# Kernel tuning notes

Measured on AMD Instinct MI355X. Metric: run time of the kernel, lower is better.

The kernel has to match this reference:

```python
import jax, jax.numpy as jnp
import numpy as np

EPS = 1e-5
K_NN = 16

def _lin1d(x, W, b):
    # 1x1 Conv1d: x (B,C,N) -> (B,O,N)
    return jnp.einsum('oc,bcn->bon', W, x) + b[None, :, None]

def _lin2d(x, W, b):
    # 1x1 Conv2d: x (B,C,N,K) -> (B,O,N,K)
    return jnp.einsum('oc,bcnk->bonk', W, x) + b[None, :, None, None]

def _bn2d(x, gamma, beta):
    # train-mode BatchNorm2d over (B, N, K) per channel
    mean = jnp.mean(x, axis=(0, 2, 3), keepdims=True)
    var = jnp.var(x, axis=(0, 2, 3), keepdims=True)
    xh = (x - mean) * jax.lax.rsqrt(var + EPS)
    return gamma[None, :, None, None] * xh + beta[None, :, None, None]

def _knn_idx(pq, ps, k):
    # pq (B,3,N), ps (B,3,M) -> idx (B,N,K) of k nearest support points
    d2 = (jnp.sum(pq * pq, axis=1)[:, :, None]
          + jnp.sum(ps * ps, axis=1)[:, None, :]
          - 2.0 * jnp.einsum('bcn,bcm->bnm', pq, ps))
    _, idx = jax.lax.top_k(-d2, k)
    return idx

def _group(x, idx):
    # x (B,C,M), idx (B,N,K) -> (B,C,N,K)
    return jnp.take_along_axis(x[:, :, None, :], idx[:, None, :, :], axis=3)

def setup_inputs() -> dict:
    key = jax.random.key(0)
    ks = jax.random.split(key, 20)
    B, C, D, N, M, H = 4, 128, 64, 2048, 2048, 256
    s = lambda k, shape, scale: (jax.random.normal(k, shape, dtype=jnp.float32) * scale)
    return {
        'pq': s(ks[0], (B, 3, N), 1.0),
        'fq': s(ks[1], (B, C, N), 1.0),
        'ps': s(ks[2], (B, 3, M), 1.0),
        'fs': s(ks[3], (B, C, M), 1.0),
        'Wq': s(ks[4], (D, C), 0.05), 'bq': jnp.zeros((D,), jnp.float32),
        'Wk': s(ks[5], (D, C), 0.05), 'bk': jnp.zeros((D,), jnp.float32),
        'Wv': s(ks[6], (D, C), 0.05), 'bv': jnp.zeros((D,), jnp.float32),
        'Wp1': s(ks[7], (D, 3), 0.2), 'bp1': jnp.zeros((D,), jnp.float32),
        'gp': jnp.ones((D,), jnp.float32), 'btp': jnp.zeros((D,), jnp.float32),
        'Wp2': s(ks[8], (D, D), 0.05), 'bp2': jnp.zeros((D,), jnp.float32),
        'Wa1': s(ks[9], (H, D), 0.05), 'ba1': jnp.zeros((H,), jnp.float32),
        'ga': jnp.ones((H,), jnp.float32), 'bta': jnp.zeros((H,), jnp.float32),
        'Wa2': s(ks[10], (D, H), 0.05), 'ba2': jnp.zeros((D,), jnp.float32),
        'We': s(ks[11], (C, D), 0.05), 'be': jnp.zeros((C,), jnp.float32),
    }

def reference(pq, fq, ps, fs, Wq, bq, Wk, bk, Wv, bv,
              Wp1, bp1, gp, btp, Wp2, bp2,
              Wa1, ba1, ga, bta, Wa2, ba2, We, be):
    identity = fq
    q = _lin1d(fq, Wq, bq)          # (B,D,N)
    k = _lin1d(fs, Wk, bk)          # (B,D,M)
    v = _lin1d(fs, Wv, bv)          # (B,D,M)
    idx = _knn_idx(pq, ps, K_NN)    # (B,N,K)
    key_g = _group(k, idx)          # (B,D,N,K)
    qk_rel = q[:, :, :, None] - key_g
    pos_rel = pq[:, :, :, None] - _group(ps, idx)  # (B,3,N,K)
    # pos_mlp: conv-bn-relu-conv
    pe = _lin2d(pos_rel, Wp1, bp1)
    pe = jax.nn.relu(_bn2d(pe, gp, btp))
    pe = _lin2d(pe, Wp2, bp2)       # (B,D,N,K)
    # attn_mlp: conv-bn-relu-conv
    a = _lin2d(qk_rel + pe, Wa1, ba1)
    a = jax.nn.relu(_bn2d(a, ga, bta))
    a = _lin2d(a, Wa2, ba2)         # (B,D,N,K)
    attn = jax.nn.softmax(a, axis=-1)
    val = _group(v, idx) + pe       # (B,D,N,K)
    agg = jnp.einsum('bcnk,bcnk->bcn', attn, val)
    return _lin1d(agg, We, be) + identity
```

## Files before the change

### kernel.cpp

```cpp
#include <hip/hip_runtime.h>
#include <stdint.h>

#define NN 2048
#define MM 2048
#define NSAMP 131072

typedef float  fv4 __attribute__((ext_vector_type(4)));
typedef short  bfv8 __attribute__((ext_vector_type(8)));
typedef short  bfv4 __attribute__((ext_vector_type(4)));
typedef unsigned short u16;
typedef unsigned long long u64;

__device__ inline u16 f2bf(float x){
  unsigned u = __float_as_uint(x);
  return (u16)((u + 0x7FFFu + ((u>>16)&1u)) >> 16);
}
__device__ inline float bf2f(u16 u){ return __uint_as_float(((unsigned)u)<<16); }
#define MFMA16 __builtin_amdgcn_mfma_f32_16x16x32_bf16

__global__ __launch_bounds__(256) void k_prep(
    const float* __restrict__ Wq, const float* __restrict__ Wk, const float* __restrict__ Wv,
    const float* __restrict__ Wp2, const float* __restrict__ Wa2, const float* __restrict__ We,
    const float* __restrict__ ps,
    u16* __restrict__ Wqbf, u16* __restrict__ Wkbf, u16* __restrict__ Wvbf,
    u16* __restrict__ Wp2bf, u16* __restrict__ Wa2bf, u16* __restrict__ Webf,
    fv4* __restrict__ psP) {
  int gid = blockIdx.x * 256 + threadIdx.x;
  if (gid < 8192)  { Wqbf[gid] = f2bf(Wq[gid]); Wkbf[gid] = f2bf(Wk[gid]);
                     Wvbf[gid] = f2bf(Wv[gid]); Webf[gid] = f2bf(We[gid]); }
  if (gid < 4096)  Wp2bf[gid] = f2bf(Wp2[gid]);
  if (gid < 16384) Wa2bf[gid] = f2bf(Wa2[gid]);
  if (gid < 8192)  { int b = gid >> 11, m = gid & 2047;
    float x = ps[(b*3+0)*MM + m], y = ps[(b*3+1)*MM + m], z = ps[(b*3+2)*MM + m];
    fv4 p; p.x = x; p.y = y; p.z = z; p.w = x*x + y*y + z*z;
    psP[gid] = p; }
}

__global__ __launch_bounds__(256) void k_qkv(
    const float* __restrict__ fq, const float* __restrict__ fs,
    const u16* __restrict__ Wqbf, const u16* __restrict__ Wkbf, const u16* __restrict__ Wvbf,
    const float* __restrict__ bq, const float* __restrict__ bk, const float* __restrict__ bv,
    float* __restrict__ qT, float* __restrict__ kT, float* __restrict__ vT) {
  __shared__ u16 tile[2][32 * 136];
  int bid = blockIdx.x;
  int b = bid >> 6, p0 = (bid & 63) * 32;
  int t = threadIdx.x;
  int w = t >> 6, l = t & 63, lq = l >> 4, ln = l & 15;
  {
    int cq = t >> 3, n4 = (t & 7) * 4;
    #pragma unroll
    for (int it = 0; it < 4; ++it) {
      int c = it * 32 + cq;
      fv4 vq = *(const fv4*)&fq[(b*128 + c)*2048 + p0 + n4];
      fv4 vs = *(const fv4*)&fs[(b*128 + c)*2048 + p0 + n4];
      #pragma unroll
      for (int j = 0; j < 4; ++j) {
        tile[0][(n4 + j)*136 + c] = f2bf(vq[j]);
        tile[1][(n4 + j)*136 + c] = f2bf(vs[j]);
      }
    }
  }
  bfv8 A[3][4];
  #pragma unroll
  for (int mat = 0; mat < 3; ++mat) {
    const u16* W = mat == 0 ? Wqbf : (mat == 1 ? Wkbf : Wvbf);
    #pragma unroll
    for (int kk = 0; kk < 4; ++kk)
      A[mat][kk] = *(const bfv8*)(W + (w*16 + ln)*128 + kk*32 + lq*8);
  }
  __syncthreads();
  fv4 acc[3][2];
  #pragma unroll
  for (int mat = 0; mat < 3; ++mat) {
    const u16* tl = tile[mat == 0 ? 0 : 1];
    #pragma unroll
    for (int nt = 0; nt < 2; ++nt) {
      fv4 a = {0.f,0.f,0.f,0.f};
      #pragma unroll
      for (int kk = 0; kk < 4; ++kk) {
        bfv8 bb = *(const bfv8*)&tl[(nt*16 + ln)*136 + kk*32 + lq*8];
        a = MFMA16(A[mat][kk], bb, a, 0, 0, 0);
      }
      acc[mat][nt] = a;
    }
  }
  #pragma unroll
  for (int mat = 0; mat < 3; ++mat) {
    float* dst = mat == 0 ? qT : (mat == 1 ? kT : vT);
    const float* bia = mat == 0 ? bq : (mat == 1 ? bk : bv);
    fv4 bq4 = *(const fv4*)&bia[w*16 + lq*4];
    #pragma unroll
    for (int nt = 0; nt < 2; ++nt) {
      fv4 o = acc[mat][nt] + bq4;
      *(fv4*)&dst[(b*NN + p0 + nt*16 + ln)*64 + w*16 + lq*4] = o;
    }
  }
}

__global__ __launch_bounds__(256) void k_knn(
    const float* __restrict__ pq, const fv4* __restrict__ psP,
    int* __restrict__ idxb, float* __restrict__ posPart) {
  __shared__ u64 list[4][512];
  __shared__ u64 win[4][16];
  __shared__ int cnt[4];
  __shared__ float sacc[4][9];

  const int t = threadIdx.x, w = t >> 6, lane = t & 63;
  const int qi = blockIdx.x * 4 + w;
  const int b = qi >> 11, n = qi & 2047;
  const float* pqb = pq + b * 3 * NN;
  const fv4* psb = psP + b * 2048;
  const float qx = pqb[n], qy = pqb[NN + n], qz = pqb[2 * NN + n];
  const float qq = qx * qx + qy * qy + qz * qz;

  unsigned key[32];
  unsigned bkey = 0xFFFFFFFFu; unsigned bj = 0;
  #pragma unroll
  for (int j = 0; j < 32; ++j) {
    fv4 P = psb[lane + 64*j];
    float d2 = qq + P.w - 2.f * (qx * P.x + qy * P.y + qz * P.z);
    unsigned bu = __float_as_uint(d2);
    bu = (bu & 0x80000000u) ? ~bu : (bu | 0x80000000u);
    key[j] = bu;
    if (bu < bkey) { bkey = bu; bj = (unsigned)j; }
  }
  u64 e = (((u64)bkey) << 32) | (unsigned)(lane + 64*(int)bj);

  #pragma unroll
  for (int k = 2; k <= 64; k <<= 1) {
    #pragma unroll
    for (int j = k >> 1; j > 0; j >>= 1) {
      u64 x = __shfl_xor(e, j, 64);
      u64 lo = e < x ? e : x, hi = e < x ? x : e;
      bool up = ((lane & k) == 0);
      bool takeLo = (((lane & j) == 0) == up);
      e = takeLo ? lo : hi;
    }
  }
  const u64 thr = __shfl(e, 15, 64);
  const unsigned T32 = (unsigned)(thr >> 32);

  if (lane == 0) cnt[w] = 0;
  #pragma unroll
  for (int j = 0; j < 32; ++j) {
    if (key[j] <= T32) {
      int p = atomicAdd(&cnt[w], 1);
      if (p < 512) list[w][p] = (((u64)key[j]) << 32) | (unsigned)(lane + 64*j);
    }
  }
  const int C = *(volatile int*)&cnt[w];

  u64 myWin = 0;
  if (C <= 64) {
    u64 v = (lane < C) ? list[w][lane] : ~0ULL;
    #pragma unroll
    for (int k = 2; k <= 64; k <<= 1) {
      #pragma unroll
      for (int j = k >> 1; j > 0; j >>= 1) {
        u64 x = __shfl_xor(v, j, 64);
        u64 lo = v < x ? v : x, hi = v < x ? x : v;
        bool up = ((lane & k) == 0);
        bool takeLo = (((lane & j) == 0) == up);
        v = takeLo ? lo : hi;
      }
    }
    myWin = v;
  } else if (C <= 128) {
    u64 e0 = list[w][lane];
    u64 e1 = (64 + lane < C) ? list[w][64 + lane] : ~0ULL;
    #pragma unroll
    for (unsigned k = 2; k <= 128; k <<= 1) {
      #pragma unroll
      for (unsigned j = k >> 1; j > 0; j >>= 1) {
        if (j < 64) {
          u64 x0 = __shfl_xor(e0, (int)j, 64);
          u64 x1 = __shfl_xor(e1, (int)j, 64);
          bool lower = ((lane & j) == 0);
          bool up0 = (k == 128) ? true : ((lane & k) == 0);
          bool up1 = (k == 128) ? true : ((k == 64) ? false : ((lane & k) == 0));
          e0 = (lower == up0) ? (e0 < x0 ? e0 : x0) : (e0 < x0 ? x0 : e0);
          e1 = (lower == up1) ? (e1 < x1 ? e1 : x1) : (e1 < x1 ? x1 : e1);
        } else {
          u64 lo = e0 < e1 ? e0 : e1, hi = e0 < e1 ? e1 : e0;
          e0 = lo; e1 = hi;
        }
      }
    }
    myWin = e0;
  } else {
    int Cc = C > 512 ? 512 : C;
    for (int i = lane; i < 512; i += 64)
      if (i >= Cc) list[w][i] = ~0ULL;
    for (int r = 0; r < 16; ++r) {
      u64 mv = ~0ULL;
      #pragma unroll
      for (int s5 = 0; s5 < 8; ++s5) {
        u64 x = list[w][s5*64 + lane];
        mv = x < mv ? x : mv;
      }
      #pragma unroll
      for (int off = 1; off <= 32; off <<= 1) {
        u64 x = __shfl_xor(mv, off, 64);
        mv = x < mv ? x : mv;
      }
      #pragma unroll
      for (int s5 = 0; s5 < 8; ++s5)
        if (list[w][s5*64 + lane] == mv) list[w][s5*64 + lane] = ~0ULL;
      if (lane == 0) win[w][r] = mv;
    }
    if (lane < 16) myWin = win[w][lane];
  }

  if (lane < 16) {
    unsigned m = (unsigned)(myWin & 0xFFFFFFFFu);
    idxb[qi * 16 + lane] = (int)m;
    fv4 P = psb[m];
    float r0 = qx - P.x, r1 = qy - P.y, r2 = qz - P.z;
    float s[9];
    s[0] = r0; s[1] = r1; s[2] = r2;
    s[3] = r0*r0; s[4] = r0*r1; s[5] = r0*r2;
    s[6] = r1*r1; s[7] = r1*r2; s[8] = r2*r2;
    #pragma unroll
    for (int off = 1; off <= 8; off <<= 1)
      #pragma unroll
      for (int i = 0; i < 9; ++i) s[i] += __shfl_xor(s[i], off, 64);
    if (lane == 0)
      #pragma unroll
      for (int i = 0; i < 9; ++i) sacc[w][i] = s[i];
  }
  __syncthreads();
  if (t < 9) posPart[blockIdx.x * 12 + t]
      = sacc[0][t] + sacc[1][t] + sacc[2][t] + sacc[3][t];
}

__global__ __launch_bounds__(256) void k_posfinal(
    const float* __restrict__ Wp1, const float* __restrict__ bp1,
    const float* __restrict__ gp, const float* __restrict__ btp,
    const float* __restrict__ posPart, float* __restrict__ Wp1f, float* __restrict__ bp1f) {
  __shared__ float red[4][9];
  __shared__ float st[9];
  int t = threadIdx.x;
  int w = t >> 6, lane = t & 63;
  float s[9];
  #pragma unroll
  for (int i = 0; i < 9; ++i) s[i] = 0.f;
  #pragma unroll
  for (int it = 0; it < 8; ++it) {
    const float* p = posPart + (it * 256 + t) * 12;
    fv4 a = *(const fv4*)p;
    fv4 b4 = *(const fv4*)(p + 4);
    float c8 = p[8];
    s[0]+=a.x; s[1]+=a.y; s[2]+=a.z; s[3]+=a.w;
    s[4]+=b4.x; s[5]+=b4.y; s[6]+=b4.z; s[7]+=b4.w;
    s[8]+=c8;
  }
  #pragma unroll
  for (int off = 32; off > 0; off >>= 1)
    #pragma unroll
    for (int i = 0; i < 9; ++i) s[i] += __shfl_xor(s[i], off, 64);
  if (lane == 0)
    #pragma unroll
    for (int i = 0; i < 9; ++i) red[w][i] = s[i];
  __syncthreads();
  if (t < 9) st[t] = red[0][t] + red[1][t] + red[2][t] + red[3][t];
  __syncthreads();
  if (t < 64) {
    int d = t;
    const float invN = 1.f / (float)NSAMP;
    float m0 = st[0]*invN, m1 = st[1]*invN, m2 = st[2]*invN;
    float C00 = st[3]*invN - m0*m0, C01 = st[4]*invN - m0*m1, C02 = st[5]*invN - m0*m2;
    float C11 = st[6]*invN - m1*m1, C12 = st[7]*invN - m1*m2, C22 = st[8]*invN - m2*m2;
    float w0 = Wp1[d*3], w1 = Wp1[d*3+1], w2 = Wp1[d*3+2];
    float mean = w0*m0 + w1*m1 + w2*m2 + bp1[d];
    float var = w0*w0*C00 + w1*w1*C11 + w2*w2*C22 + 2.f*(w0*w1*C01 + w0*w2*C02 + w1*w2*C12);
    float scale = gp[d] * rsqrtf(var + 1e-5f);
    Wp1f[d*3]   = scale * w0;
    Wp1f[d*3+1] = scale * w1;
    Wp1f[d*3+2] = scale * w2;
    bp1f[d] = btp[d] + scale * (bp1[d] - mean);
  }
}

__global__ __launch_bounds__(256) void k_ystats(
    const float* __restrict__ pq, const float* __restrict__ ps,
    const float* __restrict__ qT, const float* __restrict__ kT,
    const int* __restrict__ idxb,
    const float* __restrict__ Wp1f, const float* __restrict__ bp1f,
    const u16* __restrict__ Wp2bf, const float* __restrict__ bp2,
    float* __restrict__ Gpart, float* __restrict__ ySumPart) {
  __shared__ __align__(16) unsigned char smem[21760];
  u16*   hp   = (u16*)smem;
  u16*   y2   = (u16*)(smem + 9216);
  float* r3   = (float*)(smem + 18432);
  float* qc   = (float*)(smem + 19200);
  int*   idxA = (int*)(smem + 20224);
  float* sWp1 = (float*)(smem + 20480);
  float* sbp1 = (float*)(smem + 21248);
  float* sbp2 = (float*)(smem + 21504);

  const int t = threadIdx.x;
  const int w = t >> 6, l = t & 63, lq = l >> 4, ln = l & 15;
  const int d0 = 16*w + lq*4;

  if (t < 192) sWp1[t] = Wp1f[t];
  if (t < 64){ sbp1[t] = bp1f[t]; sbp2[t] = bp2[t]; }

  bfv8 Ape[2];
  #pragma unroll
  for (int kk = 0; kk < 2; ++kk)
    Ape[kk] = *(const bfv8*)(Wp2bf + (16*w + ln)*64 + kk*32 + lq*8);

  fv4 gacc[4];
  #pragma unroll
  for (int nt = 0; nt < 4; ++nt) gacc[nt] = (fv4){0.f,0.f,0.f,0.f};
  float ys[4] = {0.f, 0.f, 0.f, 0.f};
  __syncthreads();

  for (int ch = 0; ch < 4; ++ch) {
    const int p0 = blockIdx.x * 16 + ch * 4;
    const int b  = p0 >> 11;
    const int bN = b * 2048;
    if (t < 64) idxA[t] = idxb[p0*16 + t];
    qc[t] = qT[(p0 + (t>>6))*64 + (t & 63)];
    __syncthreads();
    if (t < 192) { int c = t >> 6, s = t & 63; int n = (p0 + (s>>4)) & 2047;
      r3[c*64 + s] = pq[(b*3+c)*NN + n] - ps[(b*3+c)*MM + idxA[s]]; }
    __syncthreads();
    { int s = t >> 2, iq = t & 3;
      float r0 = r3[s], r1 = r3[64+s], r2 = r3[128+s];
      u16 tmp[16];
      #pragma unroll
      for (int e = 0; e < 16; ++e) { int i = iq*16 + e;
        float v = sbp1[i] + sWp1[i*3]*r0 + sWp1[i*3+1]*r1 + sWp1[i*3+2]*r2;
        tmp[e] = f2bf(fmaxf(v, 0.f)); }
      *(bfv8*)&hp[s*72 + iq*16]     = *(const bfv8*)&tmp[0];
      *(bfv8*)&hp[s*72 + iq*16 + 8] = *(const bfv8*)&tmp[8];
    }
    __syncthreads();
    {
      fv4 pe[4];
      #pragma unroll
      for (int nt = 0; nt < 4; ++nt) {
        fv4 acc = {0.f,0.f,0.f,0.f};
        #pragma unroll
        for (int kk = 0; kk < 2; ++kk) {
          bfv8 bb = *(const bfv8*)&hp[(nt*16 + ln)*72 + kk*32 + lq*8];
          acc = MFMA16(Ape[kk], bb, acc, 0, 0, 0);
        }
        pe[nt] = acc;
      }
      fv4 bp2q = *(const fv4*)&sbp2[d0];
      #pragma unroll
      for (int nt = 0; nt < 4; ++nt) {
        int s = nt*16 + ln;
        int mi = idxA[s];
        fv4 kg = *(const fv4*)(kT + (bN + mi)*64 + d0);
        fv4 qv = *(const fv4*)&qc[nt*64 + d0];
        fv4 yv = qv - kg + pe[nt] + bp2q;
        #pragma unroll
        for (int r = 0; r < 4; ++r) { y2[(d0 + r)*72 + s] = f2bf(yv[r]); ys[r] += yv[r]; }
      }
    }
    __syncthreads();
    #pragma unroll
    for (int kk = 0; kk < 2; ++kk) {
      bfv8 aa = *(const bfv8*)&y2[(16*w + ln)*72 + kk*32 + lq*8];
      #pragma unroll
      for (int nt = 0; nt < 4; ++nt) {
        bfv8 bb = *(const bfv8*)&y2[(nt*16 + ln)*72 + kk*32 + lq*8];
        gacc[nt] = MFMA16(aa, bb, gacc[nt], 0, 0, 0);
      }
    }
    __syncthreads();
  }
  #pragma unroll
  for (int nt = 0; nt < 4; ++nt)
    #pragma unroll
    for (int r = 0; r < 4; ++r)
      Gpart[blockIdx.x*4096 + (16*w + lq*4 + r)*64 + nt*16 + ln] = gacc[nt][r];
  #pragma unroll
  for (int off = 1; off <= 8; off <<= 1) {
    #pragma unroll
    for (int r = 0; r < 4; ++r) ys[r] += __shfl_xor(ys[r], off, 64);
  }
  if (ln == 0) {
    #pragma unroll
    for (int r = 0; r < 4; ++r) ySumPart[blockIdx.x*64 + d0 + r] = ys[r];
  }
}

__global__ __launch_bounds__(256) void k_gred(
    const float* __restrict__ Gpart, const float* __restrict__ ySumPart,
    float* __restrict__ G, float* __restrict__ ySum) {
  __shared__ float red[256];
  int bid = blockIdx.x, t = threadIdx.x;
  int tj = t & 63, st = t >> 6;
  if (bid < 64) {
    int j = bid * 64 + tj;
    float s = 0.f;
    for (int p = st * 128; p < st * 128 + 128; ++p)
      s += Gpart[p*4096 + j];
    red[st * 64 + tj] = s;
    __syncthreads();
    if (t < 64)
      G[bid * 64 + t] = red[t] + red[64 + t] + red[128 + t] + red[192 + t];
  } else {
    float s = 0.f;
    for (int p = st * 128; p < st * 128 + 128; ++p)
      s += ySumPart[p*64 + tj];
    red[st * 64 + tj] = s;
    __syncthreads();
    if (t < 64)
      ySum[t] = red[t] + red[64 + t] + red[128 + t] + red[192 + t];
  }
}

__global__ __launch_bounds__(256) void k_attnfinal(
    const float* __restrict__ Wa1, const float* __restrict__ ba1,
    const float* __restrict__ ga, const float* __restrict__ bta,
    const float* __restrict__ ySum, const float* __restrict__ G,
    u16* __restrict__ Wa1fbf, float* __restrict__ ba1f) {
  __shared__ float red[256];
  __shared__ float mu[64];
  __shared__ float sc[1];
  int h = blockIdx.x, t = threadIdx.x;
  const float invN = 1.f / (float)NSAMP;
  if (t < 64) mu[t] = ySum[t] * invN;
  __syncthreads();
  float acc = 0.f;
  #pragma unroll
  for (int e = 0; e < 16; ++e) {
    int pi = t*16 + e, i = pi >> 6, j = pi & 63;
    float cov = G[pi]*invN - mu[i]*mu[j];
    acc += Wa1[h*64 + i] * Wa1[h*64 + j] * cov;
  }
  red[t] = acc;
  __syncthreads();
  for (int s = 128; s > 0; s >>= 1) { if (t < s) red[t] += red[t + s]; __syncthreads(); }
  float var = red[0];
  __syncthreads();
  red[t] = (t < 64) ? Wa1[h*64 + t] * mu[t] : 0.f;
  __syncthreads();
  for (int s = 128; s > 0; s >>= 1) { if (t < s) red[t] += red[t + s]; __syncthreads(); }
  if (t == 0) {
    float mean  = red[0] + ba1[h];
    float scale = ga[h] * rsqrtf(var + 1e-5f);
    sc[0] = scale;
    ba1f[h] = bta[h] + scale * (ba1[h] - mean);
  }
  __syncthreads();
  if (t < 64) Wa1fbf[h*64 + t] = f2bf(sc[0] * Wa1[h*64 + t]);
}

__global__ __launch_bounds__(256) void k_main(
    const float* __restrict__ pq, const float* __restrict__ ps,
    const float* __restrict__ qT, const float* __restrict__ kT, const float* __restrict__ vT,
    const int* __restrict__ idxb,
    const float* __restrict__ Wp1f, const float* __restrict__ bp1f,
    const u16* __restrict__ Wp2bf, const float* __restrict__ bp2,
    const u16* __restrict__ Wa1fbf, const float* __restrict__ ba1f,
    const u16* __restrict__ Wa2bf, const float* __restrict__ ba2,
    const u16* __restrict__ Webf, const float* __restrict__ be,
    const float* __restrict__ fq,
    u16* __restrict__ aggbf, float* __restrict__ out) {
  __shared__ __align__(16) unsigned char smem[65024];
  u16*   hp   = (u16*)smem;
  u16*   ha   = (u16*)smem;
  u16*   ylds = (u16*)(smem + 33792);
  float* at   = (float*)(smem + 33792);
  u16*   vt   = (u16*)(smem + 51200);
  float* r3   = (float*)(smem + 60416);
  float* qc   = (float*)(smem + 61184);
  int*   idxA = (int*)(smem + 62208);
  float* sWp1 = (float*)(smem + 62464);
  float* sbp1 = (float*)(smem + 63232);
  float* sbp2 = (float*)(smem + 63488);
  float* sba1 = (float*)(smem + 63744);
  float* sba2 = (float*)(smem + 64768);

  const int t = threadIdx.x;
  const int w = t >> 6, l = t & 63, lq = l >> 4, ln = l & 15;
  const int d0 = 16*w + lq*4;

  if (t < 192) sWp1[t] = Wp1f[t];
  if (t < 64){ sbp1[t] = bp1f[t]; sbp2[t] = bp2[t]; sba2[t] = ba2[t]; }
  sba1[t] = ba1f[t];

  bfv8 Ape[2], A1[4][2], A2[8];
  #pragma unroll
  for (int kk = 0; kk < 2; ++kk)
    Ape[kk] = *(const bfv8*)(Wp2bf + (16*w + ln)*64 + kk*32 + lq*8);
  #pragma unroll
  for (int mt = 0; mt < 4; ++mt)
    #pragma unroll
    for (int kk = 0; kk < 2; ++kk)
      A1[mt][kk] = *(const bfv8*)(Wa1fbf + (64*w + mt*16 + ln)*64 + kk*32 + lq*8);
  #pragma unroll
  for (int kk = 0; kk < 8; ++kk)
    A2[kk] = *(const bfv8*)(Wa2bf + (16*w + ln)*256 + kk*32 + lq*8);
  __syncthreads();

  for (int ch = 0; ch < 4; ++ch) {
    const int p0 = blockIdx.x * 16 + ch * 4;
    const int b  = p0 >> 11;
    const int bN = b * 2048;
    if (t < 64) idxA[t] = idxb[p0*16 + t];
    qc[t] = qT[(p0 + (t>>6))*64 + (t & 63)];
    __syncthreads();
    if (t < 192) { int c = t >> 6, s = t & 63; int n = (p0 + (s>>4)) & 2047;
      r3[c*64 + s] = pq[(b*3+c)*NN + n] - ps[(b*3+c)*MM + idxA[s]]; }
    __syncthreads();
    { int s = t >> 2, iq = t & 3;
      float r0 = r3[s], r1 = r3[64+s], r2 = r3[128+s];
      u16 tmp[16];
      #pragma unroll
      for (int e = 0; e < 16; ++e) { int i = iq*16 + e;
        float v = sbp1[i] + sWp1[i*3]*r0 + sWp1[i*3+1]*r1 + sWp1[i*3+2]*r2;
        tmp[e] = f2bf(fmaxf(v, 0.f)); }
      *(bfv8*)&hp[s*72 + iq*16]     = *(const bfv8*)&tmp[0];
      *(bfv8*)&hp[s*72 + iq*16 + 8] = *(const bfv8*)&tmp[8];
    }
    __syncthreads();
    {
      fv4 pe[4];
      #pragma unroll
      for (int nt = 0; nt < 4; ++nt) {
        fv4 acc = {0.f,0.f,0.f,0.f};
        #pragma unroll
        for (int kk = 0; kk < 2; ++kk) {
          bfv8 bb = *(const bfv8*)&hp[(nt*16 + ln)*72 + kk*32 + lq*8];
          acc = MFMA16(Ape[kk], bb, acc, 0, 0, 0);
        }
        pe[nt] = acc;
      }
      fv4 bp2q = *(const fv4*)&sbp2[d0];
      #pragma unroll
      for (int nt = 0; nt < 4; ++nt) {
        int s = nt*16 + ln;
        int mi = idxA[s];
        fv4 kg = *(const fv4*)(kT + (bN + mi)*64 + d0);
        fv4 vg = *(const fv4*)(vT + (bN + mi)*64 + d0);
        fv4 qv = *(const fv4*)&qc[nt*64 + d0];
        fv4 pv = pe[nt] + bp2q;
        fv4 yv = qv - kg + pv;
        fv4 vv = vg + pv;
        u16 yp[4], vp[4];
        #pragma unroll
        for (int r = 0; r < 4; ++r) { yp[r] = f2bf(yv[r]); vp[r] = f2bf(vv[r]); }
        *(bfv4*)&ylds[s*72 + d0] = *(const bfv4*)yp;
        *(bfv4*)&vt[s*72 + d0]   = *(const bfv4*)vp;
      }
    }
    __syncthreads();
    #pragma unroll
    for (int nt = 0; nt < 4; ++nt) {
      int s = nt*16 + ln;
      bfv8 b0 = *(const bfv8*)&ylds[s*72 + lq*8];
      bfv8 b1 = *(const bfv8*)&ylds[s*72 + 32 + lq*8];
      #pragma unroll
      for (int mt = 0; mt < 4; ++mt) {
        fv4 acc = {0.f,0.f,0.f,0.f};
        acc = MFMA16(A1[mt][0], b0, acc, 0, 0, 0);
        acc = MFMA16(A1[mt][1], b1, acc, 0, 0, 0);
        int h0 = 64*w + mt*16 + lq*4;
        fv4 bq = *(const fv4*)&sba1[h0];
        u16 hv[4];
        #pragma unroll
        for (int r = 0; r < 4; ++r) hv[r] = f2bf(fmaxf(acc[r] + bq[r], 0.f));
        *(bfv4*)&ha[s*264 + h0] = *(const bfv4*)hv;
      }
    }
    __syncthreads();
    {
      fv4 acc2[4];
      #pragma unroll
      for (int nt = 0; nt < 4; ++nt) acc2[nt] = (fv4){0.f,0.f,0.f,0.f};
      #pragma unroll
      for (int kk = 0; kk < 8; ++kk) {
        #pragma unroll
        for (int nt = 0; nt < 4; ++nt) {
          bfv8 bb = *(const bfv8*)&ha[(nt*16 + ln)*264 + kk*32 + lq*8];
          acc2[nt] = MFMA16(A2[kk], bb, acc2[nt], 0, 0, 0);
        }
      }
      fv4 ba2q = *(const fv4*)&sba2[d0];
      #pragma unroll
      for (int nt = 0; nt < 4; ++nt) {
        int s = nt*16 + ln;
        fv4 o = acc2[nt] + ba2q;
        *(fv4*)&at[s*68 + d0] = o;
      }
    }
    __syncthreads();
    {
      int dd = t & 63, pt = t >> 6;
      float a[16];
      #pragma unroll
      for (int k = 0; k < 16; ++k) a[k] = at[(pt*16 + k)*68 + dd];
      float mx = a[0];
      #pragma unroll
      for (int k = 1; k < 16; ++k) mx = fmaxf(mx, a[k]);
      float sum = 0.f, num = 0.f;
      #pragma unroll
      for (int k = 0; k < 16; ++k) {
        float e = __expf(a[k] - mx);
        sum += e;
        num += e * bf2f(vt[(pt*16 + k)*72 + dd]);
      }
      aggbf[(p0 + pt)*64 + dd] = f2bf(num / sum);
    }
    __syncthreads();
  }
  {
    const int P0 = blockIdx.x * 16;
    const int b  = P0 >> 11;
    const int n0 = P0 & 2047;
    bfv8 EA[2][2];
    #pragma unroll
    for (int mt = 0; mt < 2; ++mt)
      #pragma unroll
      for (int kk = 0; kk < 2; ++kk)
        EA[mt][kk] = *(const bfv8*)(Webf + ((w*2 + mt)*16 + ln)*64 + kk*32 + lq*8);
    const u16* bp = aggbf + (P0 + ln)*64;
    bfv8 b0 = *(const bfv8*)(bp + lq*8);
    bfv8 b1 = *(const bfv8*)(bp + 32 + lq*8);
    fv4 eacc[2];
    #pragma unroll
    for (int mt = 0; mt < 2; ++mt) {
      fv4 a = {0.f,0.f,0.f,0.f};
      a = MFMA16(EA[mt][0], b0, a, 0, 0, 0);
      a = MFMA16(EA[mt][1], b1, a, 0, 0, 0);
      eacc[mt] = a;
    }
    #pragma unroll
    for (int mt = 0; mt < 2; ++mt) {
      int c0 = (w*2 + mt)*16 + lq*4;
      fv4 bev = *(const fv4*)&be[c0];
      #pragma unroll
      for (int r = 0; r < 4; ++r) {
        int c = c0 + r;
        int o = (b*128 + c)*2048 + n0 + ln;
        out[o] = eacc[mt][r] + bev[r] + fq[o];
      }
    }
  }
}

extern "C" void kernel_launch(void* const* d_in, const int* in_sizes, int n_in,
                              void* d_out, int out_size, void* d_ws, size_t ws_size,
                              hipStream_t stream) {
  (void)in_sizes; (void)n_in; (void)out_size; (void)ws_size;
  const float* pq  = (const float*)d_in[0];
  const float* fq  = (const float*)d_in[1];
  const float* ps  = (const float*)d_in[2];
  const float* fs  = (const float*)d_in[3];
  const float* Wq  = (const float*)d_in[4];  const float* bq  = (const float*)d_in[5];
  const float* Wk  = (const float*)d_in[6];  const float* bk  = (const float*)d_in[7];
  const float* Wv  = (const float*)d_in[8];  const float* bv  = (const float*)d_in[9];
  const float* Wp1 = (const float*)d_in[10]; const float* bp1 = (const float*)d_in[11];
  const float* gp  = (const float*)d_in[12]; const float* btp = (const float*)d_in[13];
  const float* Wp2 = (const float*)d_in[14]; const float* bp2 = (const float*)d_in[15];
  const float* Wa1 = (const float*)d_in[16]; const float* ba1 = (const float*)d_in[17];
  const float* ga  = (const float*)d_in[18]; const float* bta = (const float*)d_in[19];
  const float* Wa2 = (const float*)d_in[20]; const float* ba2 = (const float*)d_in[21];
  const float* We  = (const float*)d_in[22]; const float* be  = (const float*)d_in[23];
  float* ws = (float*)d_ws;
  float* qT    = ws;
  float* kT    = ws + 524288;
  float* vT    = ws + 1048576;
  u16*   aggbf = (u16*)(ws + 1572864);
  int*   idxb  = (int*)(ws + 2097152);
  u16*   Wqbf  = (u16*)(ws + 2228224);
  u16*   Wkbf  = (u16*)(ws + 2232320);
  u16*   Wvbf  = (u16*)(ws + 2236416);
  u16*   Webf  = (u16*)(ws + 2240512);
  fv4*   psP   = (fv4*)(ws + 2244608);
  float* Wp1f  = ws + 2375680;
  float* bp1f  = ws + 2375872;
  float* ba1f  = ws + 2375936;
  float* G     = ws + 2376192;
  float* ySum  = ws + 2380288;
  float* ySumP = ws + 2380352;
  u16*   Wp2bf  = (u16*)(ws + 2413120);
  u16*   Wa2bf  = (u16*)(ws + 2415168);
  u16*   Wa1fbf = (u16*)(ws + 2423360);
  float* posPart = ws + 2431552;
  float* Gpart   = ws + 2480704;
  float* out   = (float*)d_out;

  k_prep<<<64, 256, 0, stream>>>(Wq, Wk, Wv, Wp2, Wa2, We, ps,
                                 Wqbf, Wkbf, Wvbf, Wp2bf, Wa2bf, Webf, psP);
  k_qkv<<<256, 256, 0, stream>>>(fq, fs, Wqbf, Wkbf, Wvbf, bq, bk, bv, qT, kT, vT);
  k_knn<<<2048, 256, 0, stream>>>(pq, psP, idxb, posPart);
  k_posfinal<<<1, 256, 0, stream>>>(Wp1, bp1, gp, btp, posPart, Wp1f, bp1f);
  k_ystats<<<512, 256, 0, stream>>>(pq, ps, qT, kT, idxb, Wp1f, bp1f, Wp2bf, bp2,
                                    Gpart, ySumP);
  k_gred<<<65, 256, 0, stream>>>(Gpart, ySumP, G, ySum);
  k_attnfinal<<<256, 256, 0, stream>>>(Wa1, ba1, ga, bta, ySum, G, Wa1fbf, ba1f);
  k_main<<<512, 256, 0, stream>>>(pq, ps, qT, kT, vT, idxb, Wp1f, bp1f, Wp2bf, bp2,
                                  Wa1fbf, ba1f, Wa2bf, ba2, Webf, be, fq, aggbf, out);
}
```

Measured before the change: 213.3 us.

## Materialize grouped y and value tensors in ystats; slim k_main to consume them

k_ystats now also gathers v, adds the positional encoding, and writes both the attention input y and the value tensor as bf16 to global workspace. k_main no longer recomputes the position MLP and gathers, and reads these tensors directly. It does the softmax in registers with shuffles instead of through shared memory, and uses a much smaller LDS footprint with launch bounds for higher occupancy. k_ystats runs twice as many blocks with half the points each. The trade is about 32MB of extra global write and read traffic in exchange for removing duplicated compute and LDS round trips.

```diff
diff --git a/kernel.cpp b/kernel.cpp
--- a/kernel.cpp
+++ b/kernel.cpp
@@ -283,10 +283,11 @@
 
 __global__ __launch_bounds__(256) void k_ystats(
     const float* __restrict__ pq, const float* __restrict__ ps,
-    const float* __restrict__ qT, const float* __restrict__ kT,
+    const float* __restrict__ qT, const float* __restrict__ kT, const float* __restrict__ vT,
     const int* __restrict__ idxb,
     const float* __restrict__ Wp1f, const float* __restrict__ bp1f,
     const u16* __restrict__ Wp2bf, const float* __restrict__ bp2,
+    u16* __restrict__ yg, u16* __restrict__ valg,
     float* __restrict__ Gpart, float* __restrict__ ySumPart) {
   __shared__ __align__(16) unsigned char smem[21760];
   u16*   hp   = (u16*)smem;
@@ -316,8 +317,8 @@
   float ys[4] = {0.f, 0.f, 0.f, 0.f};
   __syncthreads();
 
-  for (int ch = 0; ch < 4; ++ch) {
-    const int p0 = blockIdx.x * 16 + ch * 4;
+  for (int ch = 0; ch < 2; ++ch) {
+    const int p0 = blockIdx.x * 8 + ch * 4;
     const int b  = p0 >> 11;
     const int bN = b * 2048;
     if (t < 64) idxA[t] = idxb[p0*16 + t];
@@ -355,10 +356,20 @@
         int s = nt*16 + ln;
         int mi = idxA[s];
         fv4 kg = *(const fv4*)(kT + (bN + mi)*64 + d0);
+        fv4 vg = *(const fv4*)(vT + (bN + mi)*64 + d0);
         fv4 qv = *(const fv4*)&qc[nt*64 + d0];
-        fv4 yv = qv - kg + pe[nt] + bp2q;
+        fv4 pv = pe[nt] + bp2q;
+        fv4 yv = qv - kg + pv;
+        fv4 vv = vg + pv;
+        u16 yp[4], vp[4];
         #pragma unroll
-        for (int r = 0; r < 4; ++r) { y2[(d0 + r)*72 + s] = f2bf(yv[r]); ys[r] += yv[r]; }
+        for (int r = 0; r < 4; ++r) {
+          yp[r] = f2bf(yv[r]); vp[r] = f2bf(vv[r]);
+          y2[(d0 + r)*72 + s] = yp[r];
+          ys[r] += yv[r];
+        }
+        *(bfv4*)&yg[((u64)(p0 + nt)*16 + ln)*64 + d0]   = *(const bfv4*)yp;
+        *(bfv4*)&valg[((u64)(p0 + nt)*16 + ln)*64 + d0] = *(const bfv4*)vp;
       }
     }
     __syncthreads();
@@ -398,7 +409,7 @@
   if (bid < 64) {
     int j = bid * 64 + tj;
     float s = 0.f;
-    for (int p = st * 128; p < st * 128 + 128; ++p)
+    for (int p = st * 256; p < st * 256 + 256; ++p)
       s += Gpart[p*4096 + j];
     red[st * 64 + tj] = s;
     __syncthreads();
@@ -406,7 +417,7 @@
       G[bid * 64 + t] = red[t] + red[64 + t] + red[128 + t] + red[192 + t];
   } else {
     float s = 0.f;
-    for (int p = st * 128; p < st * 128 + 128; ++p)
+    for (int p = st * 256; p < st * 256 + 256; ++p)
       s += ySumPart[p*64 + tj];
     red[st * 64 + tj] = s;
     __syncthreads();
@@ -452,44 +463,20 @@
   if (t < 64) Wa1fbf[h*64 + t] = f2bf(sc[0] * Wa1[h*64 + t]);
 }
 
-__global__ __launch_bounds__(256) void k_main(
-    const float* __restrict__ pq, const float* __restrict__ ps,
-    const float* __restrict__ qT, const float* __restrict__ kT, const float* __restrict__ vT,
-    const int* __restrict__ idxb,
-    const float* __restrict__ Wp1f, const float* __restrict__ bp1f,
-    const u16* __restrict__ Wp2bf, const float* __restrict__ bp2,
+__global__ __launch_bounds__(256, 4) void k_main(
+    const u16* __restrict__ yg, const u16* __restrict__ valg,
     const u16* __restrict__ Wa1fbf, const float* __restrict__ ba1f,
     const u16* __restrict__ Wa2bf, const float* __restrict__ ba2,
     const u16* __restrict__ Webf, const float* __restrict__ be,
     const float* __restrict__ fq,
     u16* __restrict__ aggbf, float* __restrict__ out) {
-  __shared__ __align__(16) unsigned char smem[65024];
-  u16*   hp   = (u16*)smem;
-  u16*   ha   = (u16*)smem;
-  u16*   ylds = (u16*)(smem + 33792);
-  float* at   = (float*)(smem + 33792);
-  u16*   vt   = (u16*)(smem + 51200);
-  float* r3   = (float*)(smem + 60416);
-  float* qc   = (float*)(smem + 61184);
-  int*   idxA = (int*)(smem + 62208);
-  float* sWp1 = (float*)(smem + 62464);
-  float* sbp1 = (float*)(smem + 63232);
-  float* sbp2 = (float*)(smem + 63488);
-  float* sba1 = (float*)(smem + 63744);
-  float* sba2 = (float*)(smem + 64768);
+  __shared__ __align__(16) u16 ha[64 * 264];
 
   const int t = threadIdx.x;
   const int w = t >> 6, l = t & 63, lq = l >> 4, ln = l & 15;
   const int d0 = 16*w + lq*4;
 
-  if (t < 192) sWp1[t] = Wp1f[t];
-  if (t < 64){ sbp1[t] = bp1f[t]; sbp2[t] = bp2[t]; sba2[t] = ba2[t]; }
-  sba1[t] = ba1f[t];
-
-  bfv8 Ape[2], A1[4][2], A2[8];
-  #pragma unroll
-  for (int kk = 0; kk < 2; ++kk)
-    Ape[kk] = *(const bfv8*)(Wp2bf + (16*w + ln)*64 + kk*32 + lq*8);
+  bfv8 A1[4][2], A2[8];
   #pragma unroll
   for (int mt = 0; mt < 4; ++mt)
     #pragma unroll
@@ -498,72 +485,27 @@
   #pragma unroll
   for (int kk = 0; kk < 8; ++kk)
     A2[kk] = *(const bfv8*)(Wa2bf + (16*w + ln)*256 + kk*32 + lq*8);
-  __syncthreads();
+  fv4 bq1[4];
+  #pragma unroll
+  for (int mt = 0; mt < 4; ++mt)
+    bq1[mt] = *(const fv4*)&ba1f[64*w + mt*16 + lq*4];
+  const fv4 ba2q = *(const fv4*)&ba2[d0];
 
   for (int ch = 0; ch < 4; ++ch) {
     const int p0 = blockIdx.x * 16 + ch * 4;
-    const int b  = p0 >> 11;
-    const int bN = b * 2048;
-    if (t < 64) idxA[t] = idxb[p0*16 + t];
-    qc[t] = qT[(p0 + (t>>6))*64 + (t & 63)];
-    __syncthreads();
-    if (t < 192) { int c = t >> 6, s = t & 63; int n = (p0 + (s>>4)) & 2047;
-      r3[c*64 + s] = pq[(b*3+c)*NN + n] - ps[(b*3+c)*MM + idxA[s]]; }
-    __syncthreads();
-    { int s = t >> 2, iq = t & 3;
-      float r0 = r3[s], r1 = r3[64+s], r2 = r3[128+s];
-      u16 tmp[16];
-      #pragma unroll
-      for (int e = 0; e < 16; ++e) { int i = iq*16 + e;
-        float v = sbp1[i] + sWp1[i*3]*r0 + sWp1[i*3+1]*r1 + sWp1[i*3+2]*r2;
-        tmp[e] = f2bf(fmaxf(v, 0.f)); }
-      *(bfv8*)&hp[s*72 + iq*16]     = *(const bfv8*)&tmp[0];
-      *(bfv8*)&hp[s*72 + iq*16 + 8] = *(const bfv8*)&tmp[8];
-    }
-    __syncthreads();
-    {
-      fv4 pe[4];
-      #pragma unroll
-      for (int nt = 0; nt < 4; ++nt) {
-        fv4 acc = {0.f,0.f,0.f,0.f};
-        #pragma unroll
-        for (int kk = 0; kk < 2; ++kk) {
-          bfv8 bb = *(const bfv8*)&hp[(nt*16 + ln)*72 + kk*32 + lq*8];
-          acc = MFMA16(Ape[kk], bb, acc, 0, 0, 0);
-        }
-        pe[nt] = acc;
-      }
-      fv4 bp2q = *(const fv4*)&sbp2[d0];
-      #pragma unroll
-      for (int nt = 0; nt < 4; ++nt) {
-        int s = nt*16 + ln;
-        int mi = idxA[s];
-        fv4 kg = *(const fv4*)(kT + (bN + mi)*64 + d0);
-        fv4 vg = *(const fv4*)(vT + (bN + mi)*64 + d0);
-        fv4 qv = *(const fv4*)&qc[nt*64 + d0];
-        fv4 pv = pe[nt] + bp2q;
-        fv4 yv = qv - kg + pv;
-        fv4 vv = vg + pv;
-        u16 yp[4], vp[4];
-        #pragma unroll
-        for (int r = 0; r < 4; ++r) { yp[r] = f2bf(yv[r]); vp[r] = f2bf(vv[r]); }
-        *(bfv4*)&ylds[s*72 + d0] = *(const bfv4*)yp;
-        *(bfv4*)&vt[s*72 + d0]   = *(const bfv4*)vp;
-      }
-    }
-    __syncthreads();
     #pragma unroll
     for (int nt = 0; nt < 4; ++nt) {
+      const u16* yp = yg + ((u64)(p0 + nt)*16 + ln)*64;
+      bfv8 b0 = *(const bfv8*)(yp + lq*8);
+      bfv8 b1 = *(const bfv8*)(yp + 32 + lq*8);
       int s = nt*16 + ln;
-      bfv8 b0 = *(const bfv8*)&ylds[s*72 + lq*8];
-      bfv8 b1 = *(const bfv8*)&ylds[s*72 + 32 + lq*8];
       #pragma unroll
       for (int mt = 0; mt < 4; ++mt) {
         fv4 acc = {0.f,0.f,0.f,0.f};
         acc = MFMA16(A1[mt][0], b0, acc, 0, 0, 0);
         acc = MFMA16(A1[mt][1], b1, acc, 0, 0, 0);
         int h0 = 64*w + mt*16 + lq*4;
-        fv4 bq = *(const fv4*)&sba1[h0];
+        fv4 bq = bq1[mt];
         u16 hv[4];
         #pragma unroll
         for (int r = 0; r < 4; ++r) hv[r] = f2bf(fmaxf(acc[r] + bq[r], 0.f));
@@ -571,43 +513,46 @@
       }
     }
     __syncthreads();
-    {
-      fv4 acc2[4];
-      #pragma unroll
-      for (int nt = 0; nt < 4; ++nt) acc2[nt] = (fv4){0.f,0.f,0.f,0.f};
-      #pragma unroll
-      for (int kk = 0; kk < 8; ++kk) {
+    fv4 acc2[4];
+    #pragma unroll
+    for (int nt = 0; nt < 4; ++nt) acc2[nt] = (fv4){0.f,0.f,0.f,0.f};
+    #pragma unroll
+    for (int kk = 0; kk < 8; ++kk) {
+      #pragma unroll
+      for (int nt = 0; nt < 4; ++nt) {
+        bfv8 bb = *(const bfv8*)&ha[(nt*16 + ln)*264 + kk*32 + lq*8];
+        acc2[nt] = MFMA16(A2[kk], bb, acc2[nt], 0, 0, 0);
+      }
+    }
+    #pragma unroll
+    for (int nt = 0; nt < 4; ++nt) {
+      fv4 a = acc2[nt] + ba2q;
+      fv4 m = a;
+      #pragma unroll
+      for (int off = 1; off <= 8; off <<= 1)
         #pragma unroll
-        for (int nt = 0; nt < 4; ++nt) {
-          bfv8 bb = *(const bfv8*)&ha[(nt*16 + ln)*264 + kk*32 + lq*8];
-          acc2[nt] = MFMA16(A2[kk], bb, acc2[nt], 0, 0, 0);
+        for (int r = 0; r < 4; ++r) m[r] = fmaxf(m[r], __shfl_xor(m[r], off, 16));
+      fv4 ee, num;
+      bfv4 vv4 = *(const bfv4*)(valg + ((u64)(p0 + nt)*16 + ln)*64 + d0);
+      #pragma unroll
+      for (int r = 0; r < 4; ++r) {
+        ee[r] = __expf(a[r] - m[r]);
+        num[r] = ee[r] * bf2f((u16)vv4[r]);
+      }
+      fv4 sum = ee;
+      #pragma unroll
+      for (int off = 1; off <= 8; off <<= 1)
+        #pragma unroll
+        for (int r = 0; r < 4; ++r) {
+          sum[r] += __shfl_xor(sum[r], off, 16);
+          num[r] += __shfl_xor(num[r], off, 16);
         }
-      }
-      fv4 ba2q = *(const fv4*)&sba2[d0];
-      #pragma unroll
-      for (int nt = 0; nt < 4; ++nt) {
-        int s = nt*16 + ln;
-        fv4 o = acc2[nt] + ba2q;
-        *(fv4*)&at[s*68 + d0] = o;
-      }
-    }
-    __syncthreads();
-    {
-      int dd = t & 63, pt = t >> 6;
-      float a[16];
-      #pragma unroll
-      for (int k = 0; k < 16; ++k) a[k] = at[(pt*16 + k)*68 + dd];
-      float mx = a[0];
-      #pragma unroll
-      for (int k = 1; k < 16; ++k) mx = fmaxf(mx, a[k]);
-      float sum = 0.f, num = 0.f;
-      #pragma unroll
-      for (int k = 0; k < 16; ++k) {
-        float e = __expf(a[k] - mx);
-        sum += e;
-        num += e * bf2f(vt[(pt*16 + k)*72 + dd]);
-      }
-      aggbf[(p0 + pt)*64 + dd] = f2bf(num / sum);
+      if (ln == 0) {
+        u16 o[4];
+        #pragma unroll
+        for (int r = 0; r < 4; ++r) o[r] = f2bf(num[r] / sum[r]);
+        *(bfv4*)&aggbf[(u64)(p0 + nt)*64 + d0] = *(const bfv4*)o;
+      }
     }
     __syncthreads();
   }
@@ -669,23 +614,25 @@
   float* kT    = ws + 524288;
   float* vT    = ws + 1048576;
   u16*   aggbf = (u16*)(ws + 1572864);
-  int*   idxb  = (int*)(ws + 2097152);
-  u16*   Wqbf  = (u16*)(ws + 2228224);
-  u16*   Wkbf  = (u16*)(ws + 2232320);
-  u16*   Wvbf  = (u16*)(ws + 2236416);
-  u16*   Webf  = (u16*)(ws + 2240512);
-  fv4*   psP   = (fv4*)(ws + 2244608);
-  float* Wp1f  = ws + 2375680;
-  float* bp1f  = ws + 2375872;
-  float* ba1f  = ws + 2375936;
-  float* G     = ws + 2376192;
-  float* ySum  = ws + 2380288;
-  float* ySumP = ws + 2380352;
-  u16*   Wp2bf  = (u16*)(ws + 2413120);
-  u16*   Wa2bf  = (u16*)(ws + 2415168);
-  u16*   Wa1fbf = (u16*)(ws + 2423360);
-  float* posPart = ws + 2431552;
-  float* Gpart   = ws + 2480704;
+  int*   idxb  = (int*)(ws + 1835008);
+  u16*   Wqbf  = (u16*)(ws + 1966080);
+  u16*   Wkbf  = (u16*)(ws + 1970176);
+  u16*   Wvbf  = (u16*)(ws + 1974272);
+  u16*   Webf  = (u16*)(ws + 1978368);
+  fv4*   psP   = (fv4*)(ws + 1982464);
+  float* Wp1f  = ws + 2015232;
+  float* bp1f  = ws + 2015424;
+  float* ba1f  = ws + 2015488;
+  float* G     = ws + 2015744;
+  float* ySum  = ws + 2019840;
+  float* ySumP = ws + 2019904;
+  u16*   Wp2bf  = (u16*)(ws + 2085440);
+  u16*   Wa2bf  = (u16*)(ws + 2087488);
+  u16*   Wa1fbf = (u16*)(ws + 2095680);
+  float* posPart = ws + 2103872;
+  float* Gpart   = ws + 2128448;
+  u16*   yg    = (u16*)(ws + 6322752);
+  u16*   valg  = (u16*)(ws + 10517056);
   float* out   = (float*)d_out;
 
   k_prep<<<64, 256, 0, stream>>>(Wq, Wk, Wv, Wp2, Wa2, We, ps,
@@ -693,10 +640,10 @@
   k_qkv<<<256, 256, 0, stream>>>(fq, fs, Wqbf, Wkbf, Wvbf, bq, bk, bv, qT, kT, vT);
   k_knn<<<2048, 256, 0, stream>>>(pq, psP, idxb, posPart);
   k_posfinal<<<1, 256, 0, stream>>>(Wp1, bp1, gp, btp, posPart, Wp1f, bp1f);
-  k_ystats<<<512, 256, 0, stream>>>(pq, ps, qT, kT, idxb, Wp1f, bp1f, Wp2bf, bp2,
-                                    Gpart, ySumP);
+  k_ystats<<<1024, 256, 0, stream>>>(pq, ps, qT, kT, vT, idxb, Wp1f, bp1f, Wp2bf, bp2,
+                                     yg, valg, Gpart, ySumP);
   k_gred<<<65, 256, 0, stream>>>(Gpart, ySumP, G, ySum);
   k_attnfinal<<<256, 256, 0, stream>>>(Wa1, ba1, ga, bta, ySum, G, Wa1fbf, ba1f);
-  k_main<<<512, 256, 0, stream>>>(pq, ps, qT, kT, vT, idxb, Wp1f, bp1f, Wp2bf, bp2,
-                                  Wa1fbf, ba1f, Wa2bf, ba2, Webf, be, fq, aggbf, out);
-}
+  k_main<<<512, 256, 0, stream>>>(yg, valg, Wa1fbf, ba1f, Wa2bf, ba2, Webf, be,
+                                  fq, aggbf, out);
+}
```

Result: slower. 232.0 us (+8.8%).
